# Performance work log

Measured on AMD Instinct MI355X. Metric: run time of the kernel, lower is better.

The kernel has to match this reference:

```python
import jax, jax.numpy as jnp
import numpy as np

VOCAB = 30522
D = 768
DFF = 3072
H = 4
DQ = D // H  # 192
B, S = 4, 1024


def setup_inputs() -> dict:
    key = jax.random.key(0)
    ks = jax.random.split(key, 16)
    std = 0.02
    inp = {
        "input_ids": jax.random.randint(ks[0], (B, S), 0, VOCAB),
        "attn_mask": jnp.zeros((B, S, S), dtype=bool),
        "tok_emb": jax.random.normal(ks[1], (VOCAB, D), jnp.float32) * std,
        "seg_emb": jax.random.normal(ks[2], (VOCAB, D), jnp.float32) * std,
        "pos_emb": jax.random.normal(ks[3], (VOCAB, D), jnp.float32) * std,
        "ln_g": jnp.ones((D,), jnp.float32),
        "ln_b": jnp.zeros((D,), jnp.float32),
        # per-head projections stacked: [H, D, DQ]
        "Wq": jax.random.normal(ks[4], (H, D, DQ), jnp.float32) * std,
        "bq": jnp.zeros((H, DQ), jnp.float32),
        "Wk": jax.random.normal(ks[5], (H, D, DQ), jnp.float32) * std,
        "bk": jnp.zeros((H, DQ), jnp.float32),
        "Wv": jax.random.normal(ks[6], (H, D, DQ), jnp.float32) * std,
        "bv": jnp.zeros((H, DQ), jnp.float32),
        "Wo": jax.random.normal(ks[7], (H * DQ, D), jnp.float32) * std,
        "bo": jnp.zeros((D,), jnp.float32),
        "W1": jax.random.normal(ks[8], (D, DFF), jnp.float32) * std,
        "b1": jnp.zeros((DFF,), jnp.float32),
        "W2": jax.random.normal(ks[9], (DFF, D), jnp.float32) * std,
        "b2": jnp.zeros((D,), jnp.float32),
        "Wtok": jax.random.normal(ks[10], (D, VOCAB), jnp.float32) * std,
        "btok": jnp.zeros((VOCAB,), jnp.float32),
        "Wcls": jax.random.normal(ks[11], (D, 2), jnp.float32) * std,
        "bcls": jnp.zeros((2,), jnp.float32),
    }
    return inp


def _layer_norm(x, g, b, eps=1e-5):
    mu = jnp.mean(x, axis=-1, keepdims=True)
    var = jnp.mean((x - mu) ** 2, axis=-1, keepdims=True)
    return (x - mu) * jax.lax.rsqrt(var + eps) * g + b


def reference(input_ids, attn_mask, tok_emb, seg_emb, pos_emb, ln_g, ln_b,
              Wq, bq, Wk, bk, Wv, bv, Wo, bo, W1, b1, W2, b2,
              Wtok, btok, Wcls, bcls):
    b, s = input_ids.shape
    pos = jnp.arange(s)[None, :]  # broadcast over batch
    # NOTE: source calls embedding(input_tensor, input_tensor) -> segment uses input_ids
    x = tok_emb[input_ids] + seg_emb[input_ids] + pos_emb[pos]
    x = _layer_norm(x, ln_g, ln_b)  # [B,S,D]

    # multi-head attention (heads vectorized over H axis)
    q = jnp.einsum("bsd,hdq->bhsq", x, Wq) + bq[None, :, None, :]
    k = jnp.einsum("bsd,hdq->bhsq", x, Wk) + bk[None, :, None, :]
    v = jnp.einsum("bsd,hdq->bhsq", x, Wv) + bv[None, :, None, :]
    scale = jnp.asarray(s, x.dtype) ** 0.5  # source: query.size(1)**0.5 == sqrt(seq_len)
    scores = jnp.einsum("bhsq,bhtq->bhst", q, k) / scale
    scores = jnp.where(attn_mask[:, None, :, :], -1e9, scores)
    attn = jax.nn.softmax(scores, axis=-1)
    ctx = jnp.einsum("bhst,bhtq->bhsq", attn, v)  # [B,H,S,DQ]
    ctx = ctx.transpose(0, 2, 1, 3).reshape(b, s, H * DQ)  # concat heads in order
    attn_out = ctx @ Wo + bo

    # FFN (no residual in source; dropout is identity at eval)
    ff = jax.nn.relu(attn_out @ W1 + b1) @ W2 + b2  # [B,S,D]

    cls_out = ff[:, 0, :] @ Wcls + bcls           # [B,2]
    tok_out = ff @ Wtok + btok                    # [B,S,VOCAB]
    return cls_out, tok_out
```

## Files before the change

kernel.cpp:

```cpp
#include <hip/hip_runtime.h>
#include <hip/hip_bf16.h>
#include <cstdint>
#include <cstddef>

#define BB   4
#define SS   1024
#define DD   768
#define HH   4
#define DQ   192
#define DFF  3072
#define NVOC 30522
#define NPAD 30592

typedef __attribute__((ext_vector_type(8))) short bf16x8;
typedef __attribute__((ext_vector_type(4))) float f32x4;
#define AS1 __attribute__((address_space(1)))
#define AS3 __attribute__((address_space(3)))

static __device__ __forceinline__ float bf2f(short s) {
  union { unsigned int u; float f; } v; v.u = ((unsigned int)(unsigned short)s) << 16; return v.f;
}
static __device__ __forceinline__ short f2bf(float f) {
  union { float f; unsigned int u; } v; v.f = f;
  unsigned int r = v.u + 0x7FFFu + ((v.u >> 16) & 1u);
  if ((v.u & 0x7F800000u) == 0x7F800000u) r = v.u;
  return (short)(r >> 16);
}

__global__ __launch_bounds__(256) void k_embed_ln(
    const int* __restrict__ ids, const float* __restrict__ tok,
    const float* __restrict__ seg, const float* __restrict__ pos,
    const float* __restrict__ g, const float* __restrict__ bta,
    short* __restrict__ xb)
{
  int row = blockIdx.x;
  int s = row & (SS - 1);
  int id = ids[row];
  int t = threadIdx.x;
  const float* tp = tok + (size_t)id * DD;
  const float* sp = seg + (size_t)id * DD;
  const float* pp = pos + (size_t)s * DD;
  float v[3];
  float sum = 0.f;
#pragma unroll
  for (int j = 0; j < 3; ++j) {
    int d = t + j * 256;
    v[j] = tp[d] + sp[d] + pp[d];
    sum += v[j];
  }
  __shared__ float red[4];
#pragma unroll
  for (int w = 1; w < 64; w <<= 1) sum += __shfl_xor(sum, w);
  int wid = t >> 6, lane = t & 63;
  if (lane == 0) red[wid] = sum;
  __syncthreads();
  float mu = (red[0] + red[1] + red[2] + red[3]) * (1.f / DD);
  float vs = 0.f;
#pragma unroll
  for (int j = 0; j < 3; ++j) { float d2 = v[j] - mu; vs += d2 * d2; }
#pragma unroll
  for (int w = 1; w < 64; w <<= 1) vs += __shfl_xor(vs, w);
  __syncthreads();
  if (lane == 0) red[wid] = vs;
  __syncthreads();
  float var = (red[0] + red[1] + red[2] + red[3]) * (1.f / DD);
  float rstd = rsqrtf(var + 1e-5f);
#pragma unroll
  for (int j = 0; j < 3; ++j) {
    int d = t + j * 256;
    float val = (v[j] - mu) * rstd * g[d] + bta[d];
    xb[(size_t)row * DD + d] = f2bf(val);
  }
}

__global__ __launch_bounds__(256) void k_packqkv(
    const float* __restrict__ Wq, const float* __restrict__ Wk,
    const float* __restrict__ Wv, short* __restrict__ Bt)
{
  __shared__ float tile[32][33];
  int dq0 = blockIdx.x * 32;
  int k0  = blockIdx.y * 32;
  int z   = blockIdx.z;
  int mat = z >> 2, h = z & 3;
  const float* W = mat == 0 ? Wq : (mat == 1 ? Wk : Wv);
  int tx = threadIdx.x & 31, ty = threadIdx.x >> 5;
#pragma unroll
  for (int j = 0; j < 4; ++j) {
    int kk = ty + j * 8;
    tile[kk][tx] = W[((size_t)h * DD + k0 + kk) * DQ + dq0 + tx];
  }
  __syncthreads();
#pragma unroll
  for (int j = 0; j < 4; ++j) {
    int r = ty + j * 8;
    Bt[(size_t)(mat * DD + h * DQ + dq0 + r) * DD + k0 + tx] = f2bf(tile[tx][r]);
  }
}

__global__ void k_bpack(const float* __restrict__ bq, const float* __restrict__ bk,
                        const float* __restrict__ bv, float* __restrict__ out)
{
  int t = blockIdx.x * 256 + threadIdx.x;
  if (t >= 3 * DD) return;
  out[t] = (t < DD) ? bq[t] : (t < 2 * DD ? bk[t - DD] : bv[t - 2 * DD]);
}

__global__ __launch_bounds__(256) void k_wtrans(
    const float* __restrict__ W, short* __restrict__ Bt, int N, int K)
{
  __shared__ float tile[32][33];
  int n0 = blockIdx.x * 32, k0 = blockIdx.y * 32;
  int tx = threadIdx.x & 31, ty = threadIdx.x >> 5;
#pragma unroll
  for (int j = 0; j < 4; ++j) {
    int kk = ty + j * 8;
    tile[kk][tx] = (n0 + tx < N) ? W[(size_t)(k0 + kk) * N + n0 + tx] : 0.f;
  }
  __syncthreads();
#pragma unroll
  for (int j = 0; j < 4; ++j) {
    int r = ty + j * 8;
    Bt[(size_t)(n0 + r) * K + k0 + tx] = f2bf(tile[tx][r]);
  }
}

__global__ __launch_bounds__(256) void k_vtrans(
    const short* __restrict__ qkvb, short* __restrict__ vt)
{
  __shared__ short tile[32][33];
  int s0 = blockIdx.x * 32, d0 = blockIdx.y * 32;
  int tx = threadIdx.x & 31, ty = threadIdx.x >> 5;
#pragma unroll
  for (int j = 0; j < 4; ++j) {
    int kk = ty + j * 8;
    tile[kk][tx] = qkvb[(size_t)(s0 + kk) * 2304 + 2 * DD + d0 + tx];
  }
  __syncthreads();
#pragma unroll
  for (int j = 0; j < 4; ++j) {
    int r = ty + j * 8;
    vt[(size_t)(d0 + r) * (BB * SS) + s0 + tx] = tile[tx][r];
  }
}

template <int OUTBF, int RELU>
__global__ __launch_bounds__(256) void k_gemm_bf16(
    const short* __restrict__ A,
    const short* __restrict__ Bt,
    const float* __restrict__ bias, void* __restrict__ Cout,
    int N, int K, int NT)
{
  __shared__ alignas(16) short As[2][128 * 64];
  __shared__ alignas(16) short Bs[2][128 * 64];

  int bid = blockIdx.x;
  int xcd = bid & 7;
  int c   = bid >> 3;
  int tm  = xcd * 4 + (c & 3);
  int tn  = c >> 2;
  int m0 = tm * 128, n0 = tn * 128;

  int t = threadIdx.x;
  int w = t >> 6, l = t & 63;
  int lr = l >> 3, lc = l & 7;
  int fr = l & 15, fq = l >> 4;
  int wr = w >> 1, wc = w & 1;

  auto STAGE = [&](int buf, int k0) {
#pragma unroll
    for (int i = 0; i < 4; ++i) {
      int chunk = i * 4 + w;
      int row = chunk * 8 + lr;
      int cs = lc ^ lr;
      const short* gA = &A[(size_t)(m0 + row) * K + k0 + cs * 8];
      const short* gB = &Bt[(size_t)(n0 + row) * K + k0 + cs * 8];
      __builtin_amdgcn_global_load_lds((const AS1 void*)gA, (AS3 void*)&As[buf][chunk * 512], 16, 0, 0);
      __builtin_amdgcn_global_load_lds((const AS1 void*)gB, (AS3 void*)&Bs[buf][chunk * 512], 16, 0, 0);
    }
  };

  f32x4 acc[4][4];
#pragma unroll
  for (int i = 0; i < 4; ++i)
#pragma unroll
    for (int j = 0; j < 4; ++j)
      acc[i][j] = (f32x4){0.f, 0.f, 0.f, 0.f};

  int nk = K >> 6;
  STAGE(0, 0);
  __syncthreads();
  int cur = 0;
  for (int kt = 0; kt < nk; ++kt) {
    if (kt + 1 < nk) STAGE(cur ^ 1, (kt + 1) * 64);
    const short* Acur = &As[cur][0];
    const short* Bcur = &Bs[cur][0];
#pragma unroll
    for (int ks = 0; ks < 2; ++ks) {
      bf16x8 af[4], bfr[4];
#pragma unroll
      for (int mi = 0; mi < 4; ++mi) {
        int row = wr * 64 + mi * 16 + fr;
        int slot = (ks * 4 + fq) ^ (fr & 7);
        af[mi] = *(const bf16x8*)&Acur[row * 64 + slot * 8];
      }
#pragma unroll
      for (int nj = 0; nj < 4; ++nj) {
        int row = wc * 64 + nj * 16 + fr;
        int slot = (ks * 4 + fq) ^ (fr & 7);
        bfr[nj] = *(const bf16x8*)&Bcur[row * 64 + slot * 8];
      }
#pragma unroll
      for (int mi = 0; mi < 4; ++mi)
#pragma unroll
        for (int nj = 0; nj < 4; ++nj)
          acc[mi][nj] = __builtin_amdgcn_mfma_f32_16x16x32_bf16(af[mi], bfr[nj], acc[mi][nj], 0, 0, 0);
    }
    __syncthreads();
    cur ^= 1;
  }

#pragma unroll
  for (int nj = 0; nj < 4; ++nj) {
    int col = n0 + wc * 64 + nj * 16 + fr;
    if (col < N) {
      float bv = bias[col];
#pragma unroll
      for (int mi = 0; mi < 4; ++mi) {
#pragma unroll
        for (int rg = 0; rg < 4; ++rg) {
          int row = m0 + wr * 64 + mi * 16 + fq * 4 + rg;
          float v = acc[mi][nj][rg] + bv;
          if (RELU) v = fmaxf(v, 0.f);
          if (OUTBF) ((short*)Cout)[(size_t)row * N + col] = f2bf(v);
          else       ((float*)Cout)[(size_t)row * N + col] = v;
        }
      }
    }
  }
}

__global__ __launch_bounds__(256) void k_attn(
    const short* __restrict__ qkvb,
    const short* __restrict__ vt,
    const unsigned char* __restrict__ mask,
    float* __restrict__ opart,
    float* __restrict__ mlws)
{
  __shared__ short KsS[64 * 192];
  __shared__ short VtS[192 * 64];
  __shared__ short PsS[4 * 16 * 72];
  __shared__ unsigned char MsB[64 * 64];

  int bid = blockIdx.x;
  int x    = bid & 7;
  int r_   = bid >> 3;
  int bh   = x * 2 + (r_ & 1);
  int rest = r_ >> 1;
  int qt   = rest & 15;
  int kvh  = rest >> 4;
  int b = bh >> 2, h = bh & 3;
  int q0 = qt * 64;
  int t = threadIdx.x;
  int wq = t >> 6, l = t & 63;
  int fr = l & 15, fq = l >> 4;
  int qrow = q0 + wq * 16;

  bf16x8 qf[6];
#pragma unroll
  for (int dc = 0; dc < 6; ++dc)
    qf[dc] = *(const bf16x8*)&qkvb[(size_t)(b * SS + qrow + fr) * 2304 + h * DQ + dc * 32 + fq * 8];

  f32x4 cacc[12];
#pragma unroll
  for (int i = 0; i < 12; ++i) cacc[i] = (f32x4){0.f, 0.f, 0.f, 0.f};
  float m_r[4] = {-INFINITY, -INFINITY, -INFINITY, -INFINITY};
  float l_r[4] = {0.f, 0.f, 0.f, 0.f};

  short* myPs = &PsS[wq * 1152];

  for (int kt = kvh * 8; kt < kvh * 8 + 8; ++kt) {
    int kv0 = kt * 64;
    __syncthreads();
#pragma unroll
    for (int i = 0; i < 6; ++i) {
      int g = i * 256 + t;
      int kv = g / 24, cc = g % 24;
      int cs = cc ^ (kv & 7);
      const short* gp = &qkvb[(size_t)(b * SS + kv0 + kv) * 2304 + DD + h * DQ + cs * 8];
      __builtin_amdgcn_global_load_lds((const AS1 void*)gp, (AS3 void*)&KsS[g * 8], 16, 0, 0);
    }
#pragma unroll
    for (int i = 0; i < 6; ++i) {
      int g = i * 256 + t;
      int d = g >> 3, cc = g & 7;
      int cs = cc ^ (d & 7);
      const short* gp = &vt[(size_t)(h * DQ + d) * (BB * SS) + b * SS + kv0 + cs * 8];
      __builtin_amdgcn_global_load_lds((const AS1 void*)gp, (AS3 void*)&VtS[g * 8], 16, 0, 0);
    }
    {
      int q = t >> 2, c16 = t & 3;
      const unsigned char* gp = mask + (size_t)b * SS * SS + (size_t)(q0 + q) * SS + kv0 + c16 * 16;
      __builtin_amdgcn_global_load_lds((const AS1 void*)gp, (AS3 void*)&MsB[t * 16], 16, 0, 0);
    }
    __syncthreads();

    f32x4 s[4];
#pragma unroll
    for (int nt = 0; nt < 4; ++nt) s[nt] = (f32x4){0.f, 0.f, 0.f, 0.f};
#pragma unroll
    for (int dc = 0; dc < 6; ++dc) {
#pragma unroll
      for (int nt = 0; nt < 4; ++nt) {
        int row = nt * 16 + fr;
        int wby = (dc * 64 + fq * 16) ^ ((fr & 7) << 4);
        bf16x8 kf = *(const bf16x8*)&KsS[row * 192 + (wby >> 1)];
        s[nt] = __builtin_amdgcn_mfma_f32_16x16x32_bf16(qf[dc], kf, s[nt], 0, 0, 0);
      }
    }

    float smat[4][4];
#pragma unroll
    for (int rg = 0; rg < 4; ++rg)
#pragma unroll
      for (int nt = 0; nt < 4; ++nt) {
        float v = s[nt][rg] * (1.f / 32.f);
        if (MsB[(wq * 16 + fq * 4 + rg) * 64 + nt * 16 + fr]) v = -1e9f;
        smat[nt][rg] = v;
      }

    float svm[4];
    int ok = 1;
#pragma unroll
    for (int rg = 0; rg < 4; ++rg) {
      svm[rg] = fmaxf(fmaxf(smat[0][rg], smat[1][rg]), fmaxf(smat[2][rg], smat[3][rg]));
      ok &= (svm[rg] <= m_r[rg] + 8.f) ? 1 : 0;
    }
    float p[4][4];
    if (__all(ok)) {
#pragma unroll
      for (int rg = 0; rg < 4; ++rg)
#pragma unroll
        for (int nt = 0; nt < 4; ++nt) {
          float pv = expf(smat[nt][rg] - m_r[rg]);
          p[nt][rg] = pv;
          l_r[rg] += pv;
        }
    } else {
#pragma unroll
      for (int rg = 0; rg < 4; ++rg) {
        float mx = svm[rg];
#pragma unroll
        for (int w2 = 1; w2 < 16; w2 <<= 1) mx = fmaxf(mx, __shfl_xor(mx, w2));
        float mnew = fmaxf(m_r[rg], mx);
        float alpha = expf(m_r[rg] - mnew);
        l_r[rg] *= alpha;
#pragma unroll
        for (int nt = 0; nt < 4; ++nt) {
          float pv = expf(smat[nt][rg] - mnew);
          p[nt][rg] = pv;
          l_r[rg] += pv;
        }
#pragma unroll
        for (int nt = 0; nt < 12; ++nt) cacc[nt][rg] *= alpha;
        m_r[rg] = mnew;
      }
    }

#pragma unroll
    for (int nt = 0; nt < 4; ++nt)
#pragma unroll
      for (int rg = 0; rg < 4; ++rg)
        myPs[(fq * 4 + rg) * 72 + nt * 16 + fr] = f2bf(p[nt][rg]);
    asm volatile("s_waitcnt lgkmcnt(0)" ::: "memory");

    bf16x8 pa[2];
#pragma unroll
    for (int kc = 0; kc < 2; ++kc)
      pa[kc] = *(const bf16x8*)&myPs[fr * 72 + kc * 32 + fq * 8];
#pragma unroll
    for (int nt = 0; nt < 12; ++nt) {
      int row = nt * 16 + fr;
#pragma unroll
      for (int kc = 0; kc < 2; ++kc) {
        int wby = (kc * 64 + fq * 16) ^ ((fr & 7) << 4);
        bf16x8 vf = *(const bf16x8*)&VtS[row * 64 + (wby >> 1)];
        cacc[nt] = __builtin_amdgcn_mfma_f32_16x16x32_bf16(pa[kc], vf, cacc[nt], 0, 0, 0);
      }
    }
  }

#pragma unroll
  for (int rg = 0; rg < 4; ++rg) {
    float ls = l_r[rg];
#pragma unroll
    for (int w2 = 1; w2 < 16; w2 <<= 1) ls += __shfl_xor(ls, w2);
    l_r[rg] = ls;
  }

  float* op = opart + (size_t)kvh * (BB * SS * DD);
#pragma unroll
  for (int rg = 0; rg < 4; ++rg) {
    int row = b * SS + qrow + fq * 4 + rg;
    if (fr == 0) {
      mlws[(((size_t)kvh * (BB * SS) + row) * 4 + h) * 2 + 0] = m_r[rg];
      mlws[(((size_t)kvh * (BB * SS) + row) * 4 + h) * 2 + 1] = l_r[rg];
    }
#pragma unroll
    for (int nt = 0; nt < 12; ++nt)
      op[(size_t)row * DD + h * DQ + nt * 16 + fr] = cacc[nt][rg];
  }
}

__global__ __launch_bounds__(256) void k_amerge(
    const float* __restrict__ opart, const float* __restrict__ mlws,
    short* __restrict__ ctxb)
{
  int row = blockIdx.x;
  int t = threadIdx.x;
  __shared__ float a0s[4], a1s[4], linvs[4];
  if (t < 4) {
    float m0 = mlws[(((size_t)row) * 4 + t) * 2 + 0];
    float l0 = mlws[(((size_t)row) * 4 + t) * 2 + 1];
    float m1 = mlws[(((size_t)(BB * SS) + row) * 4 + t) * 2 + 0];
    float l1 = mlws[(((size_t)(BB * SS) + row) * 4 + t) * 2 + 1];
    float m = fmaxf(m0, m1);
    float a0 = expf(m0 - m), a1 = expf(m1 - m);
    a0s[t] = a0; a1s[t] = a1;
    linvs[t] = 1.f / (l0 * a0 + l1 * a1);
  }
  __syncthreads();
#pragma unroll
  for (int j = 0; j < 3; ++j) {
    int d = t + j * 256;
    int h = d / DQ;
    float o0 = opart[(size_t)row * DD + d];
    float o1 = opart[(size_t)(BB * SS) * DD + (size_t)row * DD + d];
    ctxb[(size_t)row * DD + d] = f2bf((o0 * a0s[h] + o1 * a1s[h]) * linvs[h]);
  }
}

__global__ void k_cls(const short* __restrict__ ffb, const float* __restrict__ Wc,
                      const float* __restrict__ bc, float* __restrict__ out)
{
  int t = threadIdx.x;
  int o = t >> 3, l8 = t & 7;
  int b = o >> 1, cN = o & 1;
  float s = 0.f;
  for (int d = l8; d < DD; d += 8)
    s += bf2f(ffb[(size_t)(b * SS) * DD + d]) * Wc[d * 2 + cN];
#pragma unroll
  for (int w = 1; w < 8; w <<= 1) s += __shfl_xor(s, w);
  if (l8 == 0) out[o] = s + bc[cN];
}

extern "C" void kernel_launch(void* const* d_in, const int* in_sizes, int n_in,
                              void* d_out, int out_size, void* d_ws, size_t ws_size,
                              hipStream_t stream)
{
  const int*           ids  = (const int*)d_in[0];
  const unsigned char* mask = (const unsigned char*)d_in[1];
  const float* tok  = (const float*)d_in[2];
  const float* seg  = (const float*)d_in[3];
  const float* pos  = (const float*)d_in[4];
  const float* ln_g = (const float*)d_in[5];
  const float* ln_b = (const float*)d_in[6];
  const float* Wq   = (const float*)d_in[7];
  const float* bq   = (const float*)d_in[8];
  const float* Wk   = (const float*)d_in[9];
  const float* bk   = (const float*)d_in[10];
  const float* Wv   = (const float*)d_in[11];
  const float* bv   = (const float*)d_in[12];
  const float* Wo   = (const float*)d_in[13];
  const float* bo   = (const float*)d_in[14];
  const float* W1   = (const float*)d_in[15];
  const float* b1   = (const float*)d_in[16];
  const float* W2   = (const float*)d_in[17];
  const float* b2   = (const float*)d_in[18];
  const float* Wtok = (const float*)d_in[19];
  const float* btok = (const float*)d_in[20];
  const float* Wcls = (const float*)d_in[21];
  const float* bcls = (const float*)d_in[22];

  float* ws = (float*)d_ws;
  short* qkvb = (short*)(ws);
  short* Bt1  = (short*)(ws);
  short* ff1b = (short*)(ws + 1310720);
  short* Btt  = (short*)(ws);
  float* opart = ws + 4718592;
  float* mlws  = ws + 4718592 + 6291456;
  short* vt   = (short*)(ws + 11747328);
  short* Btwo = (short*)(ws + 11747328);
  short* Bt2  = (short*)(ws + 11747328);
  short* ctxb = (short*)(ws + 13320192);
  short* ffb  = (short*)(ws + 13320192);
  short* xb   = (short*)(ws + 14893056);
  short* attb = (short*)(ws + 14893056);
  short* Btqkv = (short*)(ws + 16465920);
  float* bqkv = ws + 17350656;

  float* cls    = (float*)d_out;
  float* tokout = (float*)d_out + 8;

  k_embed_ln<<<BB * SS, 256, 0, stream>>>(ids, tok, seg, pos, ln_g, ln_b, xb);

  k_packqkv<<<dim3(6, 24, 12), 256, 0, stream>>>(Wq, Wk, Wv, Btqkv);
  k_bpack<<<9, 256, 0, stream>>>(bq, bk, bv, bqkv);

  k_gemm_bf16<1, 0><<<8 * 4 * 18, 256, 0, stream>>>(xb, Btqkv, bqkv, qkvb, 2304, DD, 18);

  k_vtrans<<<dim3(128, 24), 256, 0, stream>>>(qkvb, vt);

  k_attn<<<512, 256, 0, stream>>>(qkvb, vt, mask, opart, mlws);
  k_amerge<<<BB * SS, 256, 0, stream>>>(opart, mlws, ctxb);

  k_wtrans<<<dim3(24, 24), 256, 0, stream>>>(Wo, Btwo, DD, DD);
  k_gemm_bf16<1, 0><<<8 * 4 * 6, 256, 0, stream>>>(ctxb, Btwo, bo, attb, DD, DD, 6);

  k_wtrans<<<dim3(96, 24), 256, 0, stream>>>(W1, Bt1, DFF, DD);
  k_gemm_bf16<1, 1><<<8 * 4 * 24, 256, 0, stream>>>(attb, Bt1, b1, ff1b, DFF, DD, 24);
  k_wtrans<<<dim3(24, 96), 256, 0, stream>>>(W2, Bt2, DD, DFF);
  k_gemm_bf16<1, 0><<<8 * 4 * 6, 256, 0, stream>>>(ff1b, Bt2, b2, ffb, DD, DFF, 6);

  k_cls<<<1, 64, 0, stream>>>(ffb, Wcls, bcls, cls);

  k_wtrans<<<dim3(NPAD / 32, 24), 256, 0, stream>>>(Wtok, Btt, NVOC, DD);
  k_gemm_bf16<0, 0><<<8 * 4 * 239, 256, 0, stream>>>(ffb, Btt, btok, tokout, NVOC, DD, 239);
}
```

Measured before the change: 685.8 us.

## Switch GEMM to triple-buffered K=32 pipeline with explicit vmcnt waits

Restructures the bf16 GEMM main loop from double-buffered 64-wide K tiles to triple-buffered 32-wide K tiles. Loads are issued two stages ahead, and partial s_waitcnt vmcnt counts replace the full syncthreads, so global-to-LDS copies can overlap more MFMA work. The LDS swizzle is adapted to 32-element rows. This adds more barriers per unit of K and relies on exact hand-counted vmcnt values, which is fragile if the compiler emits other memory ops in the loop.

```diff
diff --git a/kernel.cpp b/kernel.cpp
--- a/kernel.cpp
+++ b/kernel.cpp
@@ -150,8 +150,8 @@
     const float* __restrict__ bias, void* __restrict__ Cout,
     int N, int K, int NT)
 {
-  __shared__ alignas(16) short As[2][128 * 64];
-  __shared__ alignas(16) short Bs[2][128 * 64];
+  __shared__ alignas(16) short As[3][128 * 32];
+  __shared__ alignas(16) short Bs[3][128 * 32];
 
   int bid = blockIdx.x;
   int xcd = bid & 7;
@@ -162,20 +162,20 @@
 
   int t = threadIdx.x;
   int w = t >> 6, l = t & 63;
-  int lr = l >> 3, lc = l & 7;
   int fr = l & 15, fq = l >> 4;
   int wr = w >> 1, wc = w & 1;
 
-  auto STAGE = [&](int buf, int k0) {
-#pragma unroll
-    for (int i = 0; i < 4; ++i) {
-      int chunk = i * 4 + w;
-      int row = chunk * 8 + lr;
-      int cs = lc ^ lr;
+  auto STAGE = [&](int buf, int kt) {
+    int k0 = kt * 32;
+#pragma unroll
+    for (int i = 0; i < 2; ++i) {
+      int G = i * 256 + t;
+      int row = G >> 2, gc = G & 3;
+      int cs = gc ^ ((row & 7) >> 1);
       const short* gA = &A[(size_t)(m0 + row) * K + k0 + cs * 8];
       const short* gB = &Bt[(size_t)(n0 + row) * K + k0 + cs * 8];
-      __builtin_amdgcn_global_load_lds((const AS1 void*)gA, (AS3 void*)&As[buf][chunk * 512], 16, 0, 0);
-      __builtin_amdgcn_global_load_lds((const AS1 void*)gB, (AS3 void*)&Bs[buf][chunk * 512], 16, 0, 0);
+      __builtin_amdgcn_global_load_lds((const AS1 void*)gA, (AS3 void*)&As[buf][G * 8], 16, 0, 0);
+      __builtin_amdgcn_global_load_lds((const AS1 void*)gB, (AS3 void*)&Bs[buf][G * 8], 16, 0, 0);
     }
   };
 
@@ -186,37 +186,41 @@
     for (int j = 0; j < 4; ++j)
       acc[i][j] = (f32x4){0.f, 0.f, 0.f, 0.f};
 
-  int nk = K >> 6;
+  int nk = K >> 5;
   STAGE(0, 0);
-  __syncthreads();
-  int cur = 0;
+  STAGE(1, 1);
+  int buf = 0;
   for (int kt = 0; kt < nk; ++kt) {
-    if (kt + 1 < nk) STAGE(cur ^ 1, (kt + 1) * 64);
-    const short* Acur = &As[cur][0];
-    const short* Bcur = &Bs[cur][0];
-#pragma unroll
-    for (int ks = 0; ks < 2; ++ks) {
-      bf16x8 af[4], bfr[4];
-#pragma unroll
-      for (int mi = 0; mi < 4; ++mi) {
-        int row = wr * 64 + mi * 16 + fr;
-        int slot = (ks * 4 + fq) ^ (fr & 7);
-        af[mi] = *(const bf16x8*)&Acur[row * 64 + slot * 8];
-      }
-#pragma unroll
-      for (int nj = 0; nj < 4; ++nj) {
-        int row = wc * 64 + nj * 16 + fr;
-        int slot = (ks * 4 + fq) ^ (fr & 7);
-        bfr[nj] = *(const bf16x8*)&Bcur[row * 64 + slot * 8];
-      }
-#pragma unroll
-      for (int mi = 0; mi < 4; ++mi)
-#pragma unroll
-        for (int nj = 0; nj < 4; ++nj)
-          acc[mi][nj] = __builtin_amdgcn_mfma_f32_16x16x32_bf16(af[mi], bfr[nj], acc[mi][nj], 0, 0, 0);
-    }
-    __syncthreads();
-    cur ^= 1;
+    if (kt + 2 < nk) {
+      STAGE((buf + 2) % 3, kt + 2);
+      asm volatile("s_waitcnt vmcnt(8)" ::: "memory");
+    } else if (kt + 1 < nk) {
+      asm volatile("s_waitcnt vmcnt(4)" ::: "memory");
+    } else {
+      asm volatile("s_waitcnt vmcnt(0)" ::: "memory");
+    }
+    __builtin_amdgcn_s_barrier();
+    const short* Acur = &As[buf][0];
+    const short* Bcur = &Bs[buf][0];
+    bf16x8 af[4], bfr[4];
+    int slot = fq ^ ((fr & 7) >> 1);
+#pragma unroll
+    for (int mi = 0; mi < 4; ++mi) {
+      int row = wr * 64 + mi * 16 + fr;
+      af[mi] = *(const bf16x8*)&Acur[row * 32 + slot * 8];
+    }
+#pragma unroll
+    for (int nj = 0; nj < 4; ++nj) {
+      int row = wc * 64 + nj * 16 + fr;
+      bfr[nj] = *(const bf16x8*)&Bcur[row * 32 + slot * 8];
+    }
+#pragma unroll
+    for (int mi = 0; mi < 4; ++mi)
+#pragma unroll
+      for (int nj = 0; nj < 4; ++nj)
+        acc[mi][nj] = __builtin_amdgcn_mfma_f32_16x16x32_bf16(af[mi], bfr[nj], acc[mi][nj], 0, 0, 0);
+    __builtin_amdgcn_s_barrier();
+    buf = (buf + 1) % 3;
   }
 
 #pragma unroll
```

Measured after the change: 667.9 us. 1.03x faster.
